# Optimization experiments

Hardware: AMD Instinct MI355X
Metric: run time of the kernel (lower is better)

## Reference

```python
import jax, jax.numpy as jnp
import numpy as np

B, C_IN, C_OUT, L = 16, 512, 512, 2048
HEADS, K, U, KS, PAD = 4, 16, 1, 3, 1
VV = C_OUT // HEADS  # 128
EPS = 1e-5


def _conv1d(x, w, pad):
    # x: [B, Cin, L], w: [Cout, Cin, KS] -> [B, Cout, L]
    return jax.lax.conv_general_dilated(
        x, w, window_strides=(1,), padding=[(pad, pad)],
        dimension_numbers=('NCH', 'OIH', 'NCH'))


def _bn_eval(y, gamma, beta, mean, var):
    # inference-mode BatchNorm1d over channel axis
    scale = gamma * jax.lax.rsqrt(var + EPS)
    shift = beta - mean * scale
    return y * scale[None, :, None] + shift[None, :, None]


def setup_inputs() -> dict:
    key = jax.random.key(0)
    ks = jax.random.split(key, 8)
    std_q = 1.0 / np.sqrt(C_IN * KS)
    x = jax.random.normal(ks[0], (B, C_IN, L), dtype=jnp.float32)
    Wq = jax.random.normal(ks[1], (K * HEADS, C_IN, KS), dtype=jnp.float32) * std_q
    Wk = jax.random.normal(ks[2], (K * U, C_IN, KS), dtype=jnp.float32) * std_q
    Wv = jax.random.normal(ks[3], (VV * U, C_IN, KS), dtype=jnp.float32) * std_q
    embedding = jax.random.normal(ks[4], (K, U), dtype=jnp.float32)
    return {
        'x': x, 'Wq': Wq,
        'q_gamma': jnp.ones((K * HEADS,), jnp.float32),
        'q_beta': jnp.zeros((K * HEADS,), jnp.float32),
        'q_mean': jnp.zeros((K * HEADS,), jnp.float32),
        'q_var': jnp.ones((K * HEADS,), jnp.float32),
        'Wk': Wk, 'Wv': Wv,
        'v_gamma': jnp.ones((VV * U,), jnp.float32),
        'v_beta': jnp.zeros((VV * U,), jnp.float32),
        'v_mean': jnp.zeros((VV * U,), jnp.float32),
        'v_var': jnp.ones((VV * U,), jnp.float32),
        'embedding': embedding,
    }


def reference(x, Wq, q_gamma, q_beta, q_mean, q_var, Wk, Wv,
              v_gamma, v_beta, v_mean, v_var, embedding):
    batch, _, n = x.shape
    # projections
    q = _bn_eval(_conv1d(x, Wq, PAD), q_gamma, q_beta, q_mean, q_var)
    q = q.reshape(batch, HEADS, K, n)                      # bhkn
    keys = _conv1d(x, Wk, PAD).reshape(batch, K, U, n)     # bkun
    sm = jax.nn.softmax(keys, axis=-1)                     # softmax over positions
    v = _bn_eval(_conv1d(x, Wv, PAD), v_gamma, v_beta, v_mean, v_var)
    v = v.reshape(batch, VV, U, n)                         # bvun
    # content lambda
    lambda_c = jnp.einsum('bkun,bvun->bkv', sm, v)
    y_c = jnp.einsum('bhkn,bkv->bhvn', q, lambda_c)
    # position lambda
    lambda_p = jnp.einsum('ku,bvun->bkvn', embedding, v)
    y_p = jnp.einsum('bhkn,bkvn->bhvn', q, lambda_p)
    out = y_c + y_p
    return out.reshape(batch, HEADS * VV, n)
```

## Files before the change

kernel.cpp:

```cpp
#include <hip/hip_runtime.h>
#include <hip/hip_bf16.h>

#define BB 16
#define CIN 512
#define LL 2048
#define HEADS 4
#define EPSV 1e-5f

typedef __attribute__((ext_vector_type(8))) short bf16x8s;
typedef __attribute__((ext_vector_type(4))) float f32x4;

__device__ __forceinline__ unsigned short f2bf(float f) {
    union { float f; unsigned int i; } c; c.f = f;
    unsigned int x = c.i;
    unsigned int lsb = (x >> 16) & 1;
    x += 0x7fff + lsb;
    return (unsigned short)(x >> 16);
}
__device__ __forceinline__ unsigned int pack2bf(float a, float b) {
    return (unsigned int)f2bf(a) | ((unsigned int)f2bf(b) << 16);
}

#define WCH_U16 7680

__global__ __launch_bounds__(256) void prep_weights(
    const float* __restrict__ Wq, const float* __restrict__ Wk,
    const float* __restrict__ Wv, unsigned short* __restrict__ Wpk)
{
    int blk = blockIdx.x;
    int cot = blk >> 4, chunk = blk & 15;
    int ci0 = chunk * 32;
    for (int i = threadIdx.x; i < WCH_U16; i += 256) {
        int t = i / 2560, r = i % 2560, co = r / 40, ci = r % 40;
        float val = 0.f;
        int cop = cot * 64 + co;
        if (ci < 32 && cop < 208) {
            int cig = ci0 + ci;
            if (cop < 64)        val = Wq[((size_t)cop * 512 + cig) * 3 + t];
            else if (cop < 80)   val = Wk[((size_t)(cop - 64) * 512 + cig) * 3 + t];
            else                 val = Wv[((size_t)(cop - 80) * 512 + cig) * 3 + t];
        }
        Wpk[(size_t)blk * WCH_U16 + i] = f2bf(val);
    }
}

#define XSTRIDE 20

__global__ __launch_bounds__(256, 2) void conv_mfma(
    const float* __restrict__ x, const unsigned short* __restrict__ Wpk,
    const float* __restrict__ qg, const float* __restrict__ qb,
    const float* __restrict__ qm, const float* __restrict__ qv,
    const float* __restrict__ vg, const float* __restrict__ vb,
    const float* __restrict__ vm, const float* __restrict__ vvar,
    float* __restrict__ qbuf, float* __restrict__ kbuf, float* __restrict__ vbuf)
{
    __shared__ __align__(16) unsigned int xT[258 * XSTRIDE];
    __shared__ __align__(16) unsigned short wA[WCH_U16];
    __shared__ float sscale[64], sshift[64];

    const int tid = threadIdx.x;
    const int wave = tid >> 6, lane = tid & 63;
    const int kq = lane >> 4, lm = lane & 15;
    const int n0 = blockIdx.x * 256;
    const int cot = blockIdx.y;
    const int b = blockIdx.z;

    if (tid < 64) {
        int cop = cot * 64 + tid;
        float sc = 1.f, sh = 0.f;
        if (cop < 64) {
            float g = qg[cop], be = qb[cop], m = qm[cop], va = qv[cop];
            sc = g * rsqrtf(va + EPSV); sh = be - m * sc;
        } else if (cop >= 80 && cop < 208) {
            int c = cop - 80;
            float g = vg[c], be = vb[c], m = vm[c], va = vvar[c];
            sc = g * rsqrtf(va + EPSV); sh = be - m * sc;
        }
        sscale[tid] = sc; sshift[tid] = sh;
    }

    f32x4 acc[4][4];
#pragma unroll
    for (int i = 0; i < 4; i++)
#pragma unroll
        for (int j = 0; j < 4; j++) acc[i][j] = (f32x4){0.f, 0.f, 0.f, 0.f};

    const float* xb = x + (size_t)b * CIN * LL;

    for (int chunk = 0; chunk < 16; chunk++) {
        __syncthreads();
        {
            const uint4* src = (const uint4*)(Wpk + (size_t)(cot * 16 + chunk) * WCH_U16);
            uint4* dst = (uint4*)wA;
            for (int i = tid; i < WCH_U16 / 8; i += 256) dst[i] = src[i];
        }
        const int ci0 = chunk * 32;
        {
            const float* xcol = xb + n0 + tid;
            unsigned int tmp[16];
#pragma unroll
            for (int p = 0; p < 16; p++) {
                float v0 = xcol[(size_t)(ci0 + 2 * p) * LL];
                float v1 = xcol[(size_t)(ci0 + 2 * p + 1) * LL];
                tmp[p] = pack2bf(v0, v1);
            }
            int row = tid + 1;
#pragma unroll
            for (int g = 0; g < 4; g++) {
                uint4 w = make_uint4(tmp[g * 4], tmp[g * 4 + 1], tmp[g * 4 + 2], tmp[g * 4 + 3]);
                *(uint4*)&xT[row * XSTRIDE + g * 4] = w;
            }
        }
        if (tid < 32) {
            int which = tid >> 4;
            int p = tid & 15;
            int gn = which ? (n0 + 256) : (n0 - 1);
            float v0 = 0.f, v1 = 0.f;
            if (gn >= 0 && gn < LL) {
                v0 = xb[(size_t)(ci0 + 2 * p) * LL + gn];
                v1 = xb[(size_t)(ci0 + 2 * p + 1) * LL + gn];
            }
            xT[(which ? 257 : 0) * XSTRIDE + p] = pack2bf(v0, v1);
        }
        __syncthreads();

#pragma unroll
        for (int t = 0; t < 3; t++) {
            bf16x8s aF[4];
#pragma unroll
            for (int cof = 0; cof < 4; cof++)
                aF[cof] = *(const bf16x8s*)&wA[((t * 4 + cof) * 16 + lm) * 40 + kq * 8];
#pragma unroll
            for (int fn = 0; fn < 4; fn++) {
                int row = wave * 64 + fn * 16 + lm + t;
                bf16x8s bF = *(const bf16x8s*)&xT[row * XSTRIDE + kq * 4];
#pragma unroll
                for (int cof = 0; cof < 4; cof++)
                    acc[cof][fn] = __builtin_amdgcn_mfma_f32_16x16x32_bf16(aF[cof], bF, acc[cof][fn], 0, 0, 0);
            }
        }
    }

#pragma unroll
    for (int cf = 0; cf < 4; cf++) {
#pragma unroll
        for (int fn = 0; fn < 4; fn++) {
#pragma unroll
            for (int r = 0; r < 4; r++) {
                int col = cf * 16 + kq * 4 + r;
                int cop = cot * 64 + col;
                if (cop >= 208) continue;
                float val = acc[cf][fn][r] * sscale[col] + sshift[col];
                int nout = n0 + wave * 64 + fn * 16 + lm;
                if (cop < 64)
                    qbuf[((size_t)b * 64 + cop) * LL + nout] = val;
                else if (cop < 80)
                    kbuf[((size_t)b * 16 + (cop - 64)) * LL + nout] = val;
                else
                    vbuf[((size_t)b * 128 + (cop - 80)) * LL + nout] = val;
            }
        }
    }
}

__global__ __launch_bounds__(256) void softmax_kernel(float* __restrict__ kbuf)
{
    const int row = blockIdx.x;
    float* p = kbuf + (size_t)row * LL;
    const int tid = threadIdx.x;
    __shared__ float red[256];

    float vals[8];
    float vmax = -1e30f;
#pragma unroll
    for (int j = 0; j < 8; j++) {
        vals[j] = p[tid + j * 256];
        vmax = fmaxf(vmax, vals[j]);
    }
    red[tid] = vmax;
    __syncthreads();
    for (int s = 128; s > 0; s >>= 1) {
        if (tid < s) red[tid] = fmaxf(red[tid], red[tid + s]);
        __syncthreads();
    }
    float m = red[0];
    __syncthreads();
    float sum = 0.f;
#pragma unroll
    for (int j = 0; j < 8; j++) {
        vals[j] = __expf(vals[j] - m);
        sum += vals[j];
    }
    red[tid] = sum;
    __syncthreads();
    for (int s = 128; s > 0; s >>= 1) {
        if (tid < s) red[tid] += red[tid + s];
        __syncthreads();
    }
    float inv = 1.f / red[0];
#pragma unroll
    for (int j = 0; j < 8; j++) p[tid + j * 256] = vals[j] * inv;
}

__global__ __launch_bounds__(256) void lambdac_kernel(
    const float* __restrict__ sm, const float* __restrict__ vbuf,
    float* __restrict__ lcT)
{
    const int wave = threadIdx.x >> 6;
    const int lane = threadIdx.x & 63;
    const int task = blockIdx.x * 4 + wave;
    const int b = task >> 6;
    const int rem = task & 63;
    const int kq4 = rem >> 4;
    const int vg = rem & 15;
    const float* ps = sm + ((size_t)b * 16 + kq4 * 4) * LL;
    const float* pv = vbuf + ((size_t)b * 128 + vg * 8) * LL;
    float acc[4][8];
#pragma unroll
    for (int ki = 0; ki < 4; ki++)
#pragma unroll
        for (int vi = 0; vi < 8; vi++) acc[ki][vi] = 0.f;

#pragma unroll 2
    for (int j = 0; j < 8; j++) {
        int n = (j * 64 + lane) * 4;
        float4 s4[4];
#pragma unroll
        for (int ki = 0; ki < 4; ki++)
            s4[ki] = *(const float4*)&ps[(size_t)ki * LL + n];
#pragma unroll
        for (int vi = 0; vi < 8; vi++) {
            float4 v4 = *(const float4*)&pv[(size_t)vi * LL + n];
#pragma unroll
            for (int ki = 0; ki < 4; ki++)
                acc[ki][vi] += s4[ki].x * v4.x + s4[ki].y * v4.y
                             + s4[ki].z * v4.z + s4[ki].w * v4.w;
        }
    }
#pragma unroll
    for (int ki = 0; ki < 4; ki++)
#pragma unroll
        for (int vi = 0; vi < 8; vi++) {
#pragma unroll
            for (int off = 32; off > 0; off >>= 1)
                acc[ki][vi] += __shfl_xor(acc[ki][vi], off, 64);
        }
    if (lane == 0) {
#pragma unroll
        for (int vi = 0; vi < 8; vi++)
#pragma unroll
            for (int ki = 0; ki < 4; ki++)
                lcT[((size_t)b * 128 + vg * 8 + vi) * 16 + kq4 * 4 + ki] = acc[ki][vi];
    }
}

__global__ __launch_bounds__(256) void final_kernel(
    const float* __restrict__ qbuf, const float* __restrict__ vbuf,
    const float* __restrict__ lcT, const float* __restrict__ emb,
    float* __restrict__ out)
{
    const int tid = threadIdx.x;
    const int n0 = blockIdx.x * 256;
    const int h = blockIdx.y;
    const int b = blockIdx.z;
    const int n = n0 + tid;

    float q[16];
    float s = 0.f;
#pragma unroll
    for (int k = 0; k < 16; k++) {
        q[k] = qbuf[((size_t)b * 64 + h * 16 + k) * LL + n];
        s += q[k] * emb[k];
    }
    const float* lcb = lcT + (size_t)b * 2048;
    const float* pv = vbuf + (size_t)b * 128 * LL + n;
    float* po = out + ((size_t)b * 512 + h * 128) * LL + n;
#pragma unroll 4
    for (int v = 0; v < 128; v++) {
        float lam = 0.f;
#pragma unroll
        for (int k = 0; k < 16; k++) lam += q[k] * lcb[v * 16 + k];
        po[(size_t)v * LL] = lam + s * pv[(size_t)v * LL];
    }
}

extern "C" void kernel_launch(void* const* d_in, const int* in_sizes, int n_in,
                              void* d_out, int out_size, void* d_ws, size_t ws_size,
                              hipStream_t stream)
{
    const float* x   = (const float*)d_in[0];
    const float* Wq  = (const float*)d_in[1];
    const float* qg  = (const float*)d_in[2];
    const float* qb  = (const float*)d_in[3];
    const float* qm  = (const float*)d_in[4];
    const float* qv  = (const float*)d_in[5];
    const float* Wk  = (const float*)d_in[6];
    const float* Wv  = (const float*)d_in[7];
    const float* vg  = (const float*)d_in[8];
    const float* vb  = (const float*)d_in[9];
    const float* vm  = (const float*)d_in[10];
    const float* vva = (const float*)d_in[11];
    const float* emb = (const float*)d_in[12];
    float* out = (float*)d_out;

    float* qbuf = (float*)d_ws;
    float* kbuf = qbuf + (size_t)BB * 64 * LL;
    float* vbuf = kbuf + (size_t)BB * 16 * LL;
    float* lcT  = vbuf + (size_t)BB * 128 * LL;
    unsigned short* Wpk = (unsigned short*)(lcT + (size_t)BB * 128 * 16);

    hipLaunchKernelGGL(prep_weights, dim3(64), dim3(256), 0, stream, Wq, Wk, Wv, Wpk);

    hipLaunchKernelGGL(conv_mfma, dim3(8, 4, 16), dim3(256), 0, stream,
                       x, Wpk, qg, qb, qm, qv, vg, vb, vm, vva,
                       qbuf, kbuf, vbuf);

    hipLaunchKernelGGL(softmax_kernel, dim3(BB * 16), dim3(256), 0, stream, kbuf);

    hipLaunchKernelGGL(lambdac_kernel, dim3(256), dim3(256), 0, stream,
                       kbuf, vbuf, lcT);

    hipLaunchKernelGGL(final_kernel, dim3(8, HEADS, BB), dim3(256), 0, stream,
                       qbuf, vbuf, lcT, emb, out);
}
```

Measured before the change: 236.3 us.

## Pipeline conv loads, shrink tiles, fuse softmax normalization into lambda kernel

The conv kernel now uses 128-wide position tiles with register-prefetched x and weight chunks, so the next chunk's global loads overlap the current chunk's MFMA work. The last output-channel tile runs only one 16-row fragment instead of padded work. Softmax no longer writes normalized keys back; a stats kernel stores the row max and inverse sum, and the lambda kernel applies exp and the scale itself. The final kernel splits the value rows across two thread halves to double the grid. This adds register pressure with launch bounds of 4 and recomputes exp inside the lambda kernel.

```diff
diff --git a/kernel.cpp b/kernel.cpp
--- a/kernel.cpp
+++ b/kernel.cpp
@@ -46,7 +46,29 @@
 
 #define XSTRIDE 20
 
-__global__ __launch_bounds__(256, 2) void conv_mfma(
+template<int NCOF>
+__device__ __forceinline__ void conv_compute(
+    const unsigned short* wA, const unsigned int* xT,
+    int wave, int lm, int kq, f32x4 acc[4][2])
+{
+#pragma unroll
+    for (int t = 0; t < 3; t++) {
+        bf16x8s aF[NCOF];
+#pragma unroll
+        for (int cof = 0; cof < NCOF; cof++)
+            aF[cof] = *(const bf16x8s*)&wA[t * 2560 + (cof * 16 + lm) * 40 + kq * 8];
+#pragma unroll
+        for (int fn = 0; fn < 2; fn++) {
+            int row = wave * 32 + fn * 16 + lm + t;
+            bf16x8s bF = *(const bf16x8s*)&xT[row * XSTRIDE + kq * 4];
+#pragma unroll
+            for (int cof = 0; cof < NCOF; cof++)
+                acc[cof][fn] = __builtin_amdgcn_mfma_f32_16x16x32_bf16(aF[cof], bF, acc[cof][fn], 0, 0, 0);
+        }
+    }
+}
+
+__global__ __launch_bounds__(256, 4) void conv_mfma(
     const float* __restrict__ x, const unsigned short* __restrict__ Wpk,
     const float* __restrict__ qg, const float* __restrict__ qb,
     const float* __restrict__ qm, const float* __restrict__ qv,
@@ -54,19 +76,20 @@
     const float* __restrict__ vm, const float* __restrict__ vvar,
     float* __restrict__ qbuf, float* __restrict__ kbuf, float* __restrict__ vbuf)
 {
-    __shared__ __align__(16) unsigned int xT[258 * XSTRIDE];
+    __shared__ __align__(16) unsigned int xT[130 * XSTRIDE];
     __shared__ __align__(16) unsigned short wA[WCH_U16];
     __shared__ float sscale[64], sshift[64];
 
     const int tid = threadIdx.x;
     const int wave = tid >> 6, lane = tid & 63;
     const int kq = lane >> 4, lm = lane & 15;
-    const int n0 = blockIdx.x * 256;
+    const int n0 = blockIdx.x * 128;
     const int cot = blockIdx.y;
     const int b = blockIdx.z;
+    const int cobase = (cot < 3) ? cot * 64 : 192;
 
     if (tid < 64) {
-        int cop = cot * 64 + tid;
+        int cop = cobase + tid;
         float sc = 1.f, sh = 0.f;
         if (cop < 64) {
             float g = qg[cop], be = qb[cop], m = qm[cop], va = qv[cop];
@@ -79,79 +102,69 @@
         sscale[tid] = sc; sshift[tid] = sh;
     }
 
-    f32x4 acc[4][4];
+    f32x4 acc[4][2];
 #pragma unroll
     for (int i = 0; i < 4; i++)
 #pragma unroll
-        for (int j = 0; j < 4; j++) acc[i][j] = (f32x4){0.f, 0.f, 0.f, 0.f};
+        for (int j = 0; j < 2; j++) acc[i][j] = (f32x4){0.f, 0.f, 0.f, 0.f};
 
     const float* xb = x + (size_t)b * CIN * LL;
-
-    for (int chunk = 0; chunk < 16; chunk++) {
+    const int srow = tid & 127;
+    const int sp8 = (tid >> 7) * 8;
+    const int hwhich = tid >> 4;
+    const int hp = tid & 15;
+
+    float xr0[8], xr1[8];
+    float hv0 = 0.f, hv1 = 0.f;
+    uint4 wr[4];
+    const uint4* wsrcb = (const uint4*)(Wpk + (size_t)cot * 16 * WCH_U16);
+
+#define LOADX(c) { int ci0 = (c) * 32; const float* xc = xb + n0 + srow;              \
+    _Pragma("unroll") for (int p = 0; p < 8; p++) {                                    \
+        xr0[p] = xc[(size_t)(ci0 + 2 * (sp8 + p)) * LL];                               \
+        xr1[p] = xc[(size_t)(ci0 + 2 * (sp8 + p) + 1) * LL]; }                         \
+    if (tid < 32) { int gn = hwhich ? (n0 + 128) : (n0 - 1);                           \
+        hv0 = 0.f; hv1 = 0.f;                                                          \
+        if (gn >= 0 && gn < LL) { hv0 = xb[(size_t)(ci0 + 2 * hp) * LL + gn];          \
+                                  hv1 = xb[(size_t)(ci0 + 2 * hp + 1) * LL + gn]; } } }
+
+#define LOADW(c) { const uint4* ws = wsrcb + (size_t)(c) * (WCH_U16 / 8);              \
+    _Pragma("unroll") for (int k = 0; k < 4; k++) {                                    \
+        int i = tid + k * 256; if (i < WCH_U16 / 8) wr[k] = ws[i]; } }
+
+#define STOREX() { unsigned int tmp[8];                                                \
+    _Pragma("unroll") for (int p = 0; p < 8; p++) tmp[p] = pack2bf(xr0[p], xr1[p]);    \
+    *(uint4*)&xT[(srow + 1) * XSTRIDE + sp8] = make_uint4(tmp[0], tmp[1], tmp[2], tmp[3]); \
+    *(uint4*)&xT[(srow + 1) * XSTRIDE + sp8 + 4] = make_uint4(tmp[4], tmp[5], tmp[6], tmp[7]); \
+    if (tid < 32) xT[(hwhich ? 129 : 0) * XSTRIDE + hp] = pack2bf(hv0, hv1); }
+
+#define STOREW() { _Pragma("unroll") for (int k = 0; k < 4; k++) {                     \
+        int i = tid + k * 256; if (i < WCH_U16 / 8) ((uint4*)wA)[i] = wr[k]; } }
+
+    LOADX(0); LOADW(0);
+    STOREX(); STOREW();
+    for (int c = 0; c < 16; c++) {
         __syncthreads();
-        {
-            const uint4* src = (const uint4*)(Wpk + (size_t)(cot * 16 + chunk) * WCH_U16);
-            uint4* dst = (uint4*)wA;
-            for (int i = tid; i < WCH_U16 / 8; i += 256) dst[i] = src[i];
-        }
-        const int ci0 = chunk * 32;
-        {
-            const float* xcol = xb + n0 + tid;
-            unsigned int tmp[16];
-#pragma unroll
-            for (int p = 0; p < 16; p++) {
-                float v0 = xcol[(size_t)(ci0 + 2 * p) * LL];
-                float v1 = xcol[(size_t)(ci0 + 2 * p + 1) * LL];
-                tmp[p] = pack2bf(v0, v1);
-            }
-            int row = tid + 1;
-#pragma unroll
-            for (int g = 0; g < 4; g++) {
-                uint4 w = make_uint4(tmp[g * 4], tmp[g * 4 + 1], tmp[g * 4 + 2], tmp[g * 4 + 3]);
-                *(uint4*)&xT[row * XSTRIDE + g * 4] = w;
-            }
-        }
-        if (tid < 32) {
-            int which = tid >> 4;
-            int p = tid & 15;
-            int gn = which ? (n0 + 256) : (n0 - 1);
-            float v0 = 0.f, v1 = 0.f;
-            if (gn >= 0 && gn < LL) {
-                v0 = xb[(size_t)(ci0 + 2 * p) * LL + gn];
-                v1 = xb[(size_t)(ci0 + 2 * p + 1) * LL + gn];
-            }
-            xT[(which ? 257 : 0) * XSTRIDE + p] = pack2bf(v0, v1);
-        }
+        if (c < 15) { LOADX(c + 1); LOADW(c + 1); }
+        if (cot < 3) conv_compute<4>(wA, xT, wave, lm, kq, acc);
+        else         conv_compute<1>(wA, xT, wave, lm, kq, acc);
         __syncthreads();
-
-#pragma unroll
-        for (int t = 0; t < 3; t++) {
-            bf16x8s aF[4];
-#pragma unroll
-            for (int cof = 0; cof < 4; cof++)
-                aF[cof] = *(const bf16x8s*)&wA[((t * 4 + cof) * 16 + lm) * 40 + kq * 8];
-#pragma unroll
-            for (int fn = 0; fn < 4; fn++) {
-                int row = wave * 64 + fn * 16 + lm + t;
-                bf16x8s bF = *(const bf16x8s*)&xT[row * XSTRIDE + kq * 4];
-#pragma unroll
-                for (int cof = 0; cof < 4; cof++)
-                    acc[cof][fn] = __builtin_amdgcn_mfma_f32_16x16x32_bf16(aF[cof], bF, acc[cof][fn], 0, 0, 0);
-            }
-        }
-    }
-
+        if (c < 15) { STOREX(); STOREW(); }
+    }
+
+    const int ncf = (cot < 3) ? 4 : 1;
 #pragma unroll
     for (int cf = 0; cf < 4; cf++) {
-#pragma unroll
-        for (int fn = 0; fn < 4; fn++) {
+        if (cf >= ncf) break;
+#pragma unroll
+        for (int fn = 0; fn < 2; fn++) {
 #pragma unroll
             for (int r = 0; r < 4; r++) {
                 int col = cf * 16 + kq * 4 + r;
-                int cop = cot * 64 + col;
+                int cop = cobase + col;
                 if (cop >= 208) continue;
                 float val = acc[cf][fn][r] * sscale[col] + sshift[col];
-                int nout = n0 + wave * 64 + fn * 16 + lm;
+                int nout = n0 + wave * 32 + fn * 16 + lm;
                 if (cop < 64)
                     qbuf[((size_t)b * 64 + cop) * LL + nout] = val;
                 else if (cop < 80)
@@ -163,10 +176,11 @@
     }
 }
 
-__global__ __launch_bounds__(256) void softmax_kernel(float* __restrict__ kbuf)
+__global__ __launch_bounds__(256) void rowstats_kernel(
+    const float* __restrict__ kbuf, float* __restrict__ stats)
 {
     const int row = blockIdx.x;
-    float* p = kbuf + (size_t)row * LL;
+    const float* p = kbuf + (size_t)row * LL;
     const int tid = threadIdx.x;
     __shared__ float red[256];
 
@@ -187,24 +201,19 @@
     __syncthreads();
     float sum = 0.f;
 #pragma unroll
-    for (int j = 0; j < 8; j++) {
-        vals[j] = __expf(vals[j] - m);
-        sum += vals[j];
-    }
+    for (int j = 0; j < 8; j++) sum += __expf(vals[j] - m);
     red[tid] = sum;
     __syncthreads();
     for (int s = 128; s > 0; s >>= 1) {
         if (tid < s) red[tid] += red[tid + s];
         __syncthreads();
     }
-    float inv = 1.f / red[0];
-#pragma unroll
-    for (int j = 0; j < 8; j++) p[tid + j * 256] = vals[j] * inv;
+    if (tid == 0) { stats[row * 2] = m; stats[row * 2 + 1] = 1.f / red[0]; }
 }
 
 __global__ __launch_bounds__(256) void lambdac_kernel(
-    const float* __restrict__ sm, const float* __restrict__ vbuf,
-    float* __restrict__ lcT)
+    const float* __restrict__ kbuf, const float* __restrict__ stats,
+    const float* __restrict__ vbuf, float* __restrict__ lcT)
 {
     const int wave = threadIdx.x >> 6;
     const int lane = threadIdx.x & 63;
@@ -213,8 +222,14 @@
     const int rem = task & 63;
     const int kq4 = rem >> 4;
     const int vg = rem & 15;
-    const float* ps = sm + ((size_t)b * 16 + kq4 * 4) * LL;
+    const float* ps = kbuf + ((size_t)b * 16 + kq4 * 4) * LL;
     const float* pv = vbuf + ((size_t)b * 128 + vg * 8) * LL;
+    float mx[4], inv[4];
+#pragma unroll
+    for (int ki = 0; ki < 4; ki++) {
+        mx[ki] = stats[(b * 16 + kq4 * 4 + ki) * 2];
+        inv[ki] = stats[(b * 16 + kq4 * 4 + ki) * 2 + 1];
+    }
     float acc[4][8];
 #pragma unroll
     for (int ki = 0; ki < 4; ki++)
@@ -226,8 +241,13 @@
         int n = (j * 64 + lane) * 4;
         float4 s4[4];
 #pragma unroll
-        for (int ki = 0; ki < 4; ki++)
-            s4[ki] = *(const float4*)&ps[(size_t)ki * LL + n];
+        for (int ki = 0; ki < 4; ki++) {
+            float4 r = *(const float4*)&ps[(size_t)ki * LL + n];
+            s4[ki].x = __expf(r.x - mx[ki]);
+            s4[ki].y = __expf(r.y - mx[ki]);
+            s4[ki].z = __expf(r.z - mx[ki]);
+            s4[ki].w = __expf(r.w - mx[ki]);
+        }
 #pragma unroll
         for (int vi = 0; vi < 8; vi++) {
             float4 v4 = *(const float4*)&pv[(size_t)vi * LL + n];
@@ -250,7 +270,8 @@
         for (int vi = 0; vi < 8; vi++)
 #pragma unroll
             for (int ki = 0; ki < 4; ki++)
-                lcT[((size_t)b * 128 + vg * 8 + vi) * 16 + kq4 * 4 + ki] = acc[ki][vi];
+                lcT[((size_t)b * 128 + vg * 8 + vi) * 16 + kq4 * 4 + ki]
+                    = acc[ki][vi] * inv[ki];
     }
 }
 
@@ -260,10 +281,11 @@
     float* __restrict__ out)
 {
     const int tid = threadIdx.x;
-    const int n0 = blockIdx.x * 256;
+    const int n0 = blockIdx.x * 128;
     const int h = blockIdx.y;
     const int b = blockIdx.z;
-    const int n = n0 + tid;
+    const int n = n0 + (tid & 127);
+    const int vh = tid >> 7;
 
     float q[16];
     float s = 0.f;
@@ -272,11 +294,11 @@
         q[k] = qbuf[((size_t)b * 64 + h * 16 + k) * LL + n];
         s += q[k] * emb[k];
     }
-    const float* lcb = lcT + (size_t)b * 2048;
-    const float* pv = vbuf + (size_t)b * 128 * LL + n;
-    float* po = out + ((size_t)b * 512 + h * 128) * LL + n;
+    const float* lcb = lcT + (size_t)b * 2048 + vh * 64 * 16;
+    const float* pv = vbuf + ((size_t)b * 128 + vh * 64) * LL + n;
+    float* po = out + ((size_t)b * 512 + h * 128 + vh * 64) * LL + n;
 #pragma unroll 4
-    for (int v = 0; v < 128; v++) {
+    for (int v = 0; v < 64; v++) {
         float lam = 0.f;
 #pragma unroll
         for (int k = 0; k < 16; k++) lam += q[k] * lcb[v * 16 + k];
@@ -307,19 +329,21 @@
     float* kbuf = qbuf + (size_t)BB * 64 * LL;
     float* vbuf = kbuf + (size_t)BB * 16 * LL;
     float* lcT  = vbuf + (size_t)BB * 128 * LL;
-    unsigned short* Wpk = (unsigned short*)(lcT + (size_t)BB * 128 * 16);
+    float* stats = lcT + (size_t)BB * 128 * 16;
+    unsigned short* Wpk = (unsigned short*)(stats + 512);
 
     hipLaunchKernelGGL(prep_weights, dim3(64), dim3(256), 0, stream, Wq, Wk, Wv, Wpk);
 
-    hipLaunchKernelGGL(conv_mfma, dim3(8, 4, 16), dim3(256), 0, stream,
+    hipLaunchKernelGGL(conv_mfma, dim3(16, 4, 16), dim3(256), 0, stream,
                        x, Wpk, qg, qb, qm, qv, vg, vb, vm, vva,
                        qbuf, kbuf, vbuf);
 
-    hipLaunchKernelGGL(softmax_kernel, dim3(BB * 16), dim3(256), 0, stream, kbuf);
+    hipLaunchKernelGGL(rowstats_kernel, dim3(BB * 16), dim3(256), 0, stream,
+                       kbuf, stats);
 
     hipLaunchKernelGGL(lambdac_kernel, dim3(256), dim3(256), 0, stream,
-                       kbuf, vbuf, lcT);
-
-    hipLaunchKernelGGL(final_kernel, dim3(8, HEADS, BB), dim3(256), 0, stream,
+                       kbuf, stats, vbuf, lcT);
+
+    hipLaunchKernelGGL(final_kernel, dim3(16, HEADS, BB), dim3(256), 0, stream,
                        qbuf, vbuf, lcT, emb, out);
 }
```

Result: slower. 300.6 us (+27.2%).
